# Kernel optimization log

Hardware: AMD Instinct MI355X
Metric: run time of the kernel (lower is better)

## Reference

```python
import jax, jax.numpy as jnp
import numpy as np

N = 50000
IN_DIM = 128
HEADS = 4
HEAD_DIM = IN_DIM // HEADS
TYPE_NUM = 3
E = 800000
NEG_SLOPE = 0.2


def setup_inputs() -> dict:
    key = jax.random.key(0)
    k1, k2, k3, k4, k5 = jax.random.split(key, 5)
    embedding = jax.random.normal(k1, (N, IN_DIM), dtype=jnp.float32)
    edges = jax.random.randint(k2, (TYPE_NUM, 2, E), 0, N, dtype=jnp.int32)
    W = jax.random.normal(k3, (TYPE_NUM, IN_DIM, HEADS, HEAD_DIM), dtype=jnp.float32) * 0.05
    a_src = jax.random.normal(k4, (TYPE_NUM, HEADS, HEAD_DIM), dtype=jnp.float32) * 0.05
    a_dst = jax.random.normal(k5, (TYPE_NUM, HEADS, HEAD_DIM), dtype=jnp.float32) * 0.05
    return {"embedding": embedding, "edges": edges, "W": W, "a_src": a_src, "a_dst": a_dst}


def _gat_layer(x, ei, W_t, asrc_t, adst_t):
    # x: [N, IN_DIM]; ei: [2, E]; W_t: [IN_DIM, H, D]
    h = jnp.einsum('nd,dhk->nhk', x, W_t)                  # [N, H, D]
    e_src = jnp.sum(h * asrc_t, axis=-1)                   # [N, H]
    e_dst = jnp.sum(h * adst_t, axis=-1)                   # [N, H]
    src, dst = ei[0], ei[1]
    e = jax.nn.leaky_relu(e_src[src] + e_dst[dst], NEG_SLOPE)  # [E, H]
    m = jax.ops.segment_max(e, dst, num_segments=N)        # [N, H]
    e = jnp.exp(e - m[dst])
    denom = jax.ops.segment_sum(e, dst, num_segments=N)    # [N, H]
    msg = h[src] * e[:, :, None]                           # [E, H, D]
    agg = jax.ops.segment_sum(msg, dst, num_segments=N)    # [N, H, D]
    out = agg / (denom[:, :, None] + 1e-9)
    return jax.nn.elu(out.reshape(N, HEADS * HEAD_DIM))


def reference(embedding, edges, W, a_src, a_dst):
    features_gat = [_gat_layer(embedding, edges[i], W[i], a_src[i], a_dst[i])
                    for i in range(TYPE_NUM)]
    # NOTE: the original module (faithfully) also uses the GAT layers for the
    # 'gcn' branch: features_gcn = [self.gat_layers[i](...) for ...]
    features_gcn = [_gat_layer(embedding, edges[i], W[i], a_src[i], a_dst[i])
                    for i in range(TYPE_NUM)]
    return (jnp.stack(features_gat), jnp.stack(features_gcn))
```

## Files before the change

kernel.cpp:

```cpp
#include <hip/hip_runtime.h>
#include <hip/hip_fp16.h>
#include <math.h>

#define NN 50000
#define IND 128
#define NH 4
#define NE 800000
#define NT 3
#define NSLOPE 0.2f

#define TILE 64
#define NBPT 782
#define NBTOT (NT * NBPT)
#define BCAP 1280

typedef _Float16 f16x8 __attribute__((ext_vector_type(8)));
typedef _Float16 f16x4 __attribute__((ext_vector_type(4)));
typedef float    f32x4 __attribute__((ext_vector_type(4)));

__global__ __launch_bounds__(256) void wt_prep_kernel(
    const float* __restrict__ W, __half* __restrict__ wt16g)
{
    int idx = blockIdx.x * 256 + threadIdx.x;
    if (idx >= NT * IND * IND) return;
    int t = idx / (IND * IND), r = idx - t * (IND * IND);
    int k = r >> 7, c = r & 127;
    wt16g[((size_t)t * IND + c) * IND + k] = (__half)W[idx];
}

__global__ __launch_bounds__(256) void gemm_mfma_kernel(
    const float* __restrict__ x, const __half* __restrict__ wt16g,
    const float* __restrict__ asrc, const float* __restrict__ adst,
    __half* __restrict__ h16, float* __restrict__ es, float* __restrict__ ed)
{
    __shared__ __align__(16) __half tile[4][16 * 136];
    const int t = blockIdx.y;
    const int tid = threadIdx.x;
    const int wid = tid >> 6, lane = tid & 63;
    const int l15 = lane & 15, l4 = lane >> 4;
    const int r0 = blockIdx.x * 64 + wid * 16;
    const bool active = (r0 < NN);

    const __half* wt = wt16g + (size_t)t * IND * IND;
    const float* xrow = x + (size_t)((active ? r0 : 0) + l15) * IND;

    f32x4 acc[8];
    #pragma unroll
    for (int i = 0; i < 8; i++) acc[i] = (f32x4){0.f, 0.f, 0.f, 0.f};

    #pragma unroll
    for (int ks = 0; ks < 4; ks++) {
        const int kb = ks * 32 + l4 * 8;
        float4 x0 = *reinterpret_cast<const float4*>(xrow + kb);
        float4 x1 = *reinterpret_cast<const float4*>(xrow + kb + 4);
        f16x8 af;
        af[0] = (_Float16)x0.x; af[1] = (_Float16)x0.y;
        af[2] = (_Float16)x0.z; af[3] = (_Float16)x0.w;
        af[4] = (_Float16)x1.x; af[5] = (_Float16)x1.y;
        af[6] = (_Float16)x1.z; af[7] = (_Float16)x1.w;
        #pragma unroll
        for (int ct = 0; ct < 8; ct++) {
            f16x8 bf = *reinterpret_cast<const f16x8*>(wt + (size_t)(ct * 16 + l15) * IND + kb);
            acc[ct] = __builtin_amdgcn_mfma_f32_16x16x32_f16(af, bf, acc[ct], 0, 0, 0);
        }
    }

    __half* tl = tile[wid];
    #pragma unroll
    for (int ct = 0; ct < 8; ct++)
        #pragma unroll
        for (int r = 0; r < 4; r++)
            tl[(l4 * 4 + r) * 136 + ct * 16 + l15] = (__half)acc[ct][r];
    __syncthreads();

    if (active) {
        #pragma unroll
        for (int i = 0; i < 4; i++) {
            int c = lane + 64 * i;
            int row = c >> 4, off = (c & 15) * 8;
            f16x8 v = *reinterpret_cast<const f16x8*>(tl + row * 136 + off);
            *reinterpret_cast<f16x8*>(h16 + ((size_t)t * NN + r0 + row) * IND + off) = v;
        }
        int row16 = lane >> 2, head = lane & 3;
        const __half* hr = tl + row16 * 136 + head * 32;
        const float* av = asrc + ((size_t)t * NH + head) * 32;
        const float* bv = adst + ((size_t)t * NH + head) * 32;
        float se = 0.f, de = 0.f;
        #pragma unroll
        for (int jj = 0; jj < 4; jj++) {
            f16x8 hv = *reinterpret_cast<const f16x8*>(hr + jj * 8);
            #pragma unroll
            for (int j = 0; j < 8; j++) {
                float hf = (float)hv[j];
                se = fmaf(hf, av[jj * 8 + j], se);
                de = fmaf(hf, bv[jj * 8 + j], de);
            }
        }
        int n = r0 + row16;
        es[((size_t)t * NN + n) * NH + head] = se;
        ed[((size_t)t * NN + n) * NH + head] = de;
    }
}

__global__ __launch_bounds__(256) void init_gcursor_kernel(int* __restrict__ gcursor)
{
    int i = blockIdx.x * 256 + threadIdx.x;
    if (i < NBTOT) gcursor[i] = i * BCAP;
}

__global__ __launch_bounds__(512) void bucket_scatter_kernel(
    const int* __restrict__ edges, int* __restrict__ gcursor, unsigned* __restrict__ bucketed)
{
    __shared__ int cnt[NBTOT];
    __shared__ int base[NBTOT];
    const int tid = threadIdx.x;
    for (int i = tid; i < NBTOT; i += 512) cnt[i] = 0;
    __syncthreads();
    const long long gtot = (long long)NT * NE;
    const long long g0 = (long long)blockIdx.x * 8192;
    long long g1 = g0 + 8192; if (g1 > gtot) g1 = gtot;
    for (long long g = g0 + tid; g < g1; g += 512) {
        int t = (g >= 2LL * NE) ? 2 : (g >= NE ? 1 : 0);
        int e = (int)(g - (long long)t * NE);
        int d = edges[(size_t)t * 2 * NE + NE + e];
        atomicAdd(&cnt[t * NBPT + (d >> 6)], 1);
    }
    __syncthreads();
    for (int i = tid; i < NBTOT; i += 512) {
        int c = cnt[i];
        base[i] = c ? atomicAdd(&gcursor[i], c) : 0;
        cnt[i] = 0;
    }
    __syncthreads();
    for (long long g = g0 + tid; g < g1; g += 512) {
        int t = (g >= 2LL * NE) ? 2 : (g >= NE ? 1 : 0);
        int e = (int)(g - (long long)t * NE);
        const int* eb = edges + (size_t)t * 2 * NE;
        int s = eb[e], d = eb[NE + e];
        int bg = t * NBPT + (d >> 6);
        int pos = base[bg] + atomicAdd(&cnt[bg], 1);
        bucketed[pos] = (unsigned)s | ((unsigned)(d & 63) << 16);
    }
}

__global__ __launch_bounds__(512) void bucket_sort_kernel(
    unsigned* __restrict__ bucketed, const int* __restrict__ gcursor,
    int* __restrict__ begA, int* __restrict__ endA)
{
    __shared__ unsigned pk[BCAP];
    __shared__ unsigned srt[BCAP];
    __shared__ int hist[TILE];
    __shared__ int scn[TILE];
    __shared__ int cur[TILE];
    const int bg = blockIdx.x;
    const int tid = threadIdx.x;
    const int base = bg * BCAP;
    const int cnt = gcursor[bg] - base;
    if (tid < TILE) { hist[tid] = 0; cur[tid] = 0; }
    __syncthreads();
    for (int i = tid; i < cnt; i += 512) {
        unsigned v = bucketed[base + i];
        pk[i] = v;
        atomicAdd(&hist[(v >> 16) & 63u], 1);
    }
    __syncthreads();
    if (tid < 64) {
        int v = hist[tid];
        int inc = v;
        #pragma unroll
        for (int off = 1; off < 64; off <<= 1) {
            int n = __shfl_up(inc, off, 64);
            if (tid >= off) inc += n;
        }
        scn[tid] = inc - v;
    }
    __syncthreads();
    for (int i = tid; i < cnt; i += 512) {
        unsigned v = pk[i];
        int dl = (int)((v >> 16) & 63u);
        int pos = scn[dl] + atomicAdd(&cur[dl], 1);
        srt[pos] = v & 0xFFFFu;
    }
    __syncthreads();
    for (int i = tid; i < cnt; i += 512) bucketed[base + i] = srt[i];
    if (tid < 64) {
        int t = bg / NBPT;
        int node = (bg - t * NBPT) * TILE + tid;
        if (node < NN) {
            int g = t * NN + node;
            begA[g] = base + scn[tid];
            endA[g] = base + scn[tid] + hist[tid];
        }
    }
}

__global__ __launch_bounds__(256) void gat_fused_kernel(
    const int* __restrict__ begA, const int* __restrict__ endA,
    const unsigned* __restrict__ ssrc,
    const float* __restrict__ es, const float* __restrict__ ed,
    const __half* __restrict__ h16,
    float* __restrict__ out)
{
    const int g = blockIdx.x * 4 + (threadIdx.x >> 6);
    if (g >= NT * NN) return;
    const int lane = threadIdx.x & 63;
    const int t = g / NN;
    const int dst = g - t * NN;
    const int beg = begA[g], end = endA[g];
    const int el = lane >> 5, dl = lane & 31;
    const int hsel = dl >> 3;
    const float* es_t = es + (size_t)t * NN * NH;
    const float edv = ed[(size_t)g * NH + (lane & 3)];
    const __half* h16_t = h16 + (size_t)t * NN * IND;

    float a0 = 0.f, a1 = 0.f, a2 = 0.f, a3 = 0.f, dsum = 0.f;

    for (int base = beg; base < end; base += 16) {
        int ne = end - base; if (ne > 16) ne = 16;
        const int ei = lane >> 2;
        float wv = 0.f; int sv = 0;
        if (ei < ne) {
            sv = (int)ssrc[base + ei];
            float s = es_t[(sv << 2) + (lane & 3)] + edv;
            s = s > 0.f ? s : NSLOPE * s;
            wv = __expf(s);
            dsum += wv;
        }
        int kk = 0;
        for (; kk + 2 <= ne; kk += 2) {
            int k2 = kk + el;
            int   sb = __shfl(sv, k2 << 2, 64);
            float wb = __shfl(wv, (k2 << 2) | hsel, 64);
            f16x4 hv = *reinterpret_cast<const f16x4*>(h16_t + ((size_t)sb << 7) + (dl << 2));
            a0 = fmaf(wb, (float)hv[0], a0);
            a1 = fmaf(wb, (float)hv[1], a1);
            a2 = fmaf(wb, (float)hv[2], a2);
            a3 = fmaf(wb, (float)hv[3], a3);
        }
        if (kk < ne) {
            int   sb = __shfl(sv, kk << 2, 64);
            float wb = __shfl(wv, (kk << 2) | hsel, 64);
            if (el == 0) {
                f16x4 hv = *reinterpret_cast<const f16x4*>(h16_t + ((size_t)sb << 7) + (dl << 2));
                a0 = fmaf(wb, (float)hv[0], a0);
                a1 = fmaf(wb, (float)hv[1], a1);
                a2 = fmaf(wb, (float)hv[2], a2);
                a3 = fmaf(wb, (float)hv[3], a3);
            }
        }
    }

    #pragma unroll
    for (int m = 4; m <= 32; m <<= 1) dsum += __shfl_xor(dsum, m, 64);
    a0 += __shfl_xor(a0, 32, 64);
    a1 += __shfl_xor(a1, 32, 64);
    a2 += __shfl_xor(a2, 32, 64);
    a3 += __shfl_xor(a3, 32, 64);
    float dn = __shfl(dsum, hsel, 64) + 1e-9f;

    if (el == 0) {
        float v0 = a0 / dn, v1 = a1 / dn, v2 = a2 / dn, v3 = a3 / dn;
        f32x4 o;
        o[0] = v0 > 0.f ? v0 : expm1f(v0);
        o[1] = v1 > 0.f ? v1 : expm1f(v1);
        o[2] = v2 > 0.f ? v2 : expm1f(v2);
        o[3] = v3 > 0.f ? v3 : expm1f(v3);
        float* obase = out + (size_t)t * NN * IND + ((size_t)dst << 7) + (dl << 2);
        __builtin_nontemporal_store(o, reinterpret_cast<f32x4*>(obase));
        __builtin_nontemporal_store(o, reinterpret_cast<f32x4*>(obase + (size_t)NT * NN * IND));
    }
}

extern "C" void kernel_launch(void* const* d_in, const int* in_sizes, int n_in,
                              void* d_out, int out_size, void* d_ws, size_t ws_size,
                              hipStream_t stream)
{
    const float* x     = (const float*)d_in[0];
    const int*   edges = (const int*)d_in[1];
    const float* W     = (const float*)d_in[2];
    const float* asrc  = (const float*)d_in[3];
    const float* adst  = (const float*)d_in[4];
    float* out = (float*)d_out;

    char* p = (char*)d_ws;
    __half*   h16      = (__half*)p;   p += (size_t)NT * NN * IND * 2;
    float*    es       = (float*)p;    p += (size_t)NT * NN * NH * 4;
    float*    ed       = (float*)p;    p += (size_t)NT * NN * NH * 4;
    int*      gcursor  = (int*)p;      p += (size_t)NBTOT * 4;
    int*      begA     = (int*)p;      p += (size_t)NT * NN * 4;
    int*      endA     = (int*)p;      p += (size_t)NT * NN * 4;
    __half*   wt16g    = (__half*)p;   p += (size_t)NT * IND * IND * 2;
    unsigned* bucketed = (unsigned*)p; p += ((size_t)NBTOT * BCAP + 1024) * 4;

    wt_prep_kernel<<<(NT * IND * IND + 255) / 256, 256, 0, stream>>>(W, wt16g);
    init_gcursor_kernel<<<(NBTOT + 255) / 256, 256, 0, stream>>>(gcursor);
    bucket_scatter_kernel<<<(NT * NE + 8191) / 8192, 512, 0, stream>>>(edges, gcursor, bucketed);
    bucket_sort_kernel<<<NBTOT, 512, 0, stream>>>(bucketed, gcursor, begA, endA);

    dim3 ggrid((NN + 63) / 64, NT);
    gemm_mfma_kernel<<<ggrid, 256, 0, stream>>>(x, wt16g, asrc, adst, h16, es, ed);

    gat_fused_kernel<<<(NT * NN + 3) / 4, 256, 0, stream>>>(
        begA, endA, bucketed, es, ed, h16, out);
}
```

Baseline: 247.5 us.

## Fuse kernels: merge prep, run scatter alongside GEMM, sort-and-aggregate per bucket

Cuts the launch count from six to three. Weight prep and cursor init now share one kernel. The edge bucket scatter and the MFMA GEMM run as disjoint block ranges of a single launch, so they can overlap. The bucket sort is fused with the GAT aggregation, so sorted source indices stay in LDS and no begin/end arrays are written or read back from global memory. The aggregation also uses inline v_fma_mix_f32 to fold the fp16-to-fp32 conversion into the FMA. In exchange, each 512-thread block now processes 64 destination nodes serially, eight per wave, which may reduce parallelism and hurt load balance on degree-skewed buckets.

```diff
diff --git a/kernel.cpp b/kernel.cpp
--- a/kernel.cpp
+++ b/kernel.cpp
@@ -14,31 +14,74 @@
 #define NBTOT (NT * NBPT)
 #define BCAP 1280
 
+#define SCB ((NT * NE + 8191) / 8192)
+#define GXB ((NN + 127) / 128)
+
 typedef _Float16 f16x8 __attribute__((ext_vector_type(8)));
-typedef _Float16 f16x4 __attribute__((ext_vector_type(4)));
 typedef float    f32x4 __attribute__((ext_vector_type(4)));
 
-__global__ __launch_bounds__(256) void wt_prep_kernel(
-    const float* __restrict__ W, __half* __restrict__ wt16g)
+__global__ __launch_bounds__(256) void prep_kernel(
+    const float* __restrict__ W, __half* __restrict__ wt16g, int* __restrict__ gcursor)
 {
     int idx = blockIdx.x * 256 + threadIdx.x;
-    if (idx >= NT * IND * IND) return;
-    int t = idx / (IND * IND), r = idx - t * (IND * IND);
-    int k = r >> 7, c = r & 127;
-    wt16g[((size_t)t * IND + c) * IND + k] = (__half)W[idx];
-}
-
-__global__ __launch_bounds__(256) void gemm_mfma_kernel(
+    if (idx < NT * IND * IND) {
+        int t = idx / (IND * IND), r = idx - t * (IND * IND);
+        int k = r >> 7, c = r & 127;
+        wt16g[((size_t)t * IND + c) * IND + k] = (__half)W[idx];
+    }
+    if (idx < NBTOT) gcursor[idx] = idx * BCAP;
+}
+
+__global__ __launch_bounds__(512) void scatter_gemm_kernel(
+    const int* __restrict__ edges, int* __restrict__ gcursor, unsigned* __restrict__ bucketed,
     const float* __restrict__ x, const __half* __restrict__ wt16g,
     const float* __restrict__ asrc, const float* __restrict__ adst,
     __half* __restrict__ h16, float* __restrict__ es, float* __restrict__ ed)
 {
-    __shared__ __align__(16) __half tile[4][16 * 136];
-    const int t = blockIdx.y;
+    __shared__ __align__(16) char ldsbuf[34816];
     const int tid = threadIdx.x;
+
+    if (blockIdx.x < SCB) {
+        int* cnt = (int*)ldsbuf;
+        int* bas = cnt + NBTOT;
+        for (int i = tid; i < NBTOT; i += 512) cnt[i] = 0;
+        __syncthreads();
+        const long long gtot = (long long)NT * NE;
+        const long long g0 = (long long)blockIdx.x * 8192;
+        long long g1 = g0 + 8192; if (g1 > gtot) g1 = gtot;
+        for (long long g = g0 + tid; g < g1; g += 512) {
+            int t = (g >= 2LL * NE) ? 2 : (g >= NE ? 1 : 0);
+            int e = (int)(g - (long long)t * NE);
+            int d = edges[(size_t)t * 2 * NE + NE + e];
+            atomicAdd(&cnt[t * NBPT + (d >> 6)], 1);
+        }
+        __syncthreads();
+        for (int i = tid; i < NBTOT; i += 512) {
+            int c = cnt[i];
+            bas[i] = c ? atomicAdd(&gcursor[i], c) : 0;
+            cnt[i] = 0;
+        }
+        __syncthreads();
+        for (long long g = g0 + tid; g < g1; g += 512) {
+            int t = (g >= 2LL * NE) ? 2 : (g >= NE ? 1 : 0);
+            int e = (int)(g - (long long)t * NE);
+            const int* eb = edges + (size_t)t * 2 * NE;
+            int s = eb[e], d = eb[NE + e];
+            int bg = t * NBPT + (d >> 6);
+            int pos = bas[bg] + atomicAdd(&cnt[bg], 1);
+            bucketed[pos] = (unsigned)s | ((unsigned)(d & 63) << 16);
+        }
+        return;
+    }
+
+    const int bx = blockIdx.x - SCB;
+    const int t  = bx / GXB;
+    const int gx = bx - t * GXB;
+    __half* tile = (__half*)ldsbuf;
     const int wid = tid >> 6, lane = tid & 63;
+    __half* tl = tile + wid * (16 * 136);
     const int l15 = lane & 15, l4 = lane >> 4;
-    const int r0 = blockIdx.x * 64 + wid * 16;
+    const int r0 = gx * 128 + wid * 16;
     const bool active = (r0 < NN);
 
     const __half* wt = wt16g + (size_t)t * IND * IND;
@@ -65,7 +108,6 @@
         }
     }
 
-    __half* tl = tile[wid];
     #pragma unroll
     for (int ct = 0; ct < 8; ct++)
         #pragma unroll
@@ -102,60 +144,21 @@
     }
 }
 
-__global__ __launch_bounds__(256) void init_gcursor_kernel(int* __restrict__ gcursor)
-{
-    int i = blockIdx.x * 256 + threadIdx.x;
-    if (i < NBTOT) gcursor[i] = i * BCAP;
-}
-
-__global__ __launch_bounds__(512) void bucket_scatter_kernel(
-    const int* __restrict__ edges, int* __restrict__ gcursor, unsigned* __restrict__ bucketed)
-{
-    __shared__ int cnt[NBTOT];
-    __shared__ int base[NBTOT];
-    const int tid = threadIdx.x;
-    for (int i = tid; i < NBTOT; i += 512) cnt[i] = 0;
-    __syncthreads();
-    const long long gtot = (long long)NT * NE;
-    const long long g0 = (long long)blockIdx.x * 8192;
-    long long g1 = g0 + 8192; if (g1 > gtot) g1 = gtot;
-    for (long long g = g0 + tid; g < g1; g += 512) {
-        int t = (g >= 2LL * NE) ? 2 : (g >= NE ? 1 : 0);
-        int e = (int)(g - (long long)t * NE);
-        int d = edges[(size_t)t * 2 * NE + NE + e];
-        atomicAdd(&cnt[t * NBPT + (d >> 6)], 1);
-    }
-    __syncthreads();
-    for (int i = tid; i < NBTOT; i += 512) {
-        int c = cnt[i];
-        base[i] = c ? atomicAdd(&gcursor[i], c) : 0;
-        cnt[i] = 0;
-    }
-    __syncthreads();
-    for (long long g = g0 + tid; g < g1; g += 512) {
-        int t = (g >= 2LL * NE) ? 2 : (g >= NE ? 1 : 0);
-        int e = (int)(g - (long long)t * NE);
-        const int* eb = edges + (size_t)t * 2 * NE;
-        int s = eb[e], d = eb[NE + e];
-        int bg = t * NBPT + (d >> 6);
-        int pos = base[bg] + atomicAdd(&cnt[bg], 1);
-        bucketed[pos] = (unsigned)s | ((unsigned)(d & 63) << 16);
-    }
-}
-
-__global__ __launch_bounds__(512) void bucket_sort_kernel(
-    unsigned* __restrict__ bucketed, const int* __restrict__ gcursor,
-    int* __restrict__ begA, int* __restrict__ endA)
+__global__ __launch_bounds__(512) void gat_bucket_kernel(
+    const unsigned* __restrict__ bucketed, const int* __restrict__ gcursor,
+    const float* __restrict__ es, const float* __restrict__ ed,
+    const __half* __restrict__ h16, float* __restrict__ out)
 {
     __shared__ unsigned pk[BCAP];
     __shared__ unsigned srt[BCAP];
-    __shared__ int hist[TILE];
-    __shared__ int scn[TILE];
-    __shared__ int cur[TILE];
+    __shared__ int hist[TILE], scn[TILE], cur[TILE];
     const int bg = blockIdx.x;
+    const int t = bg / NBPT;
+    const int node0 = (bg - t * NBPT) * TILE;
     const int tid = threadIdx.x;
     const int base = bg * BCAP;
     const int cnt = gcursor[bg] - base;
+
     if (tid < TILE) { hist[tid] = 0; cur[tid] = 0; }
     __syncthreads();
     for (int i = tid; i < cnt; i += 512) {
@@ -182,92 +185,76 @@
         srt[pos] = v & 0xFFFFu;
     }
     __syncthreads();
-    for (int i = tid; i < cnt; i += 512) bucketed[base + i] = srt[i];
-    if (tid < 64) {
-        int t = bg / NBPT;
-        int node = (bg - t * NBPT) * TILE + tid;
-        if (node < NN) {
-            int g = t * NN + node;
-            begA[g] = base + scn[tid];
-            endA[g] = base + scn[tid] + hist[tid];
-        }
-    }
-}
-
-__global__ __launch_bounds__(256) void gat_fused_kernel(
-    const int* __restrict__ begA, const int* __restrict__ endA,
-    const unsigned* __restrict__ ssrc,
-    const float* __restrict__ es, const float* __restrict__ ed,
-    const __half* __restrict__ h16,
-    float* __restrict__ out)
-{
-    const int g = blockIdx.x * 4 + (threadIdx.x >> 6);
-    if (g >= NT * NN) return;
-    const int lane = threadIdx.x & 63;
-    const int t = g / NN;
-    const int dst = g - t * NN;
-    const int beg = begA[g], end = endA[g];
-    const int el = lane >> 5, dl = lane & 31;
-    const int hsel = dl >> 3;
+
+    const int wid = tid >> 6, lane = tid & 63;
+    const int el = lane >> 5, dl2 = lane & 31;
+    const int hsel = dl2 >> 3;
     const float* es_t = es + (size_t)t * NN * NH;
-    const float edv = ed[(size_t)g * NH + (lane & 3)];
     const __half* h16_t = h16 + (size_t)t * NN * IND;
 
-    float a0 = 0.f, a1 = 0.f, a2 = 0.f, a3 = 0.f, dsum = 0.f;
-
-    for (int base = beg; base < end; base += 16) {
-        int ne = end - base; if (ne > 16) ne = 16;
-        const int ei = lane >> 2;
-        float wv = 0.f; int sv = 0;
-        if (ei < ne) {
-            sv = (int)ssrc[base + ei];
-            float s = es_t[(sv << 2) + (lane & 3)] + edv;
-            s = s > 0.f ? s : NSLOPE * s;
-            wv = __expf(s);
-            dsum += wv;
-        }
-        int kk = 0;
-        for (; kk + 2 <= ne; kk += 2) {
-            int k2 = kk + el;
-            int   sb = __shfl(sv, k2 << 2, 64);
-            float wb = __shfl(wv, (k2 << 2) | hsel, 64);
-            f16x4 hv = *reinterpret_cast<const f16x4*>(h16_t + ((size_t)sb << 7) + (dl << 2));
-            a0 = fmaf(wb, (float)hv[0], a0);
-            a1 = fmaf(wb, (float)hv[1], a1);
-            a2 = fmaf(wb, (float)hv[2], a2);
-            a3 = fmaf(wb, (float)hv[3], a3);
-        }
-        if (kk < ne) {
-            int   sb = __shfl(sv, kk << 2, 64);
-            float wb = __shfl(wv, (kk << 2) | hsel, 64);
-            if (el == 0) {
-                f16x4 hv = *reinterpret_cast<const f16x4*>(h16_t + ((size_t)sb << 7) + (dl << 2));
-                a0 = fmaf(wb, (float)hv[0], a0);
-                a1 = fmaf(wb, (float)hv[1], a1);
-                a2 = fmaf(wb, (float)hv[2], a2);
-                a3 = fmaf(wb, (float)hv[3], a3);
-            }
-        }
-    }
-
-    #pragma unroll
-    for (int m = 4; m <= 32; m <<= 1) dsum += __shfl_xor(dsum, m, 64);
-    a0 += __shfl_xor(a0, 32, 64);
-    a1 += __shfl_xor(a1, 32, 64);
-    a2 += __shfl_xor(a2, 32, 64);
-    a3 += __shfl_xor(a3, 32, 64);
-    float dn = __shfl(dsum, hsel, 64) + 1e-9f;
-
-    if (el == 0) {
-        float v0 = a0 / dn, v1 = a1 / dn, v2 = a2 / dn, v3 = a3 / dn;
-        f32x4 o;
-        o[0] = v0 > 0.f ? v0 : expm1f(v0);
-        o[1] = v1 > 0.f ? v1 : expm1f(v1);
-        o[2] = v2 > 0.f ? v2 : expm1f(v2);
-        o[3] = v3 > 0.f ? v3 : expm1f(v3);
-        float* obase = out + (size_t)t * NN * IND + ((size_t)dst << 7) + (dl << 2);
-        __builtin_nontemporal_store(o, reinterpret_cast<f32x4*>(obase));
-        __builtin_nontemporal_store(o, reinterpret_cast<f32x4*>(obase + (size_t)NT * NN * IND));
+    for (int j = 0; j < 8; j++) {
+        const int dloc = wid * 8 + j;
+        const int node = node0 + dloc;
+        if (node >= NN) break;
+        const int beg = scn[dloc], nE = hist[dloc];
+        const float edv = ed[((size_t)t * NN + node) * NH + (lane & 3)];
+
+        float a0 = 0.f, a1 = 0.f, a2 = 0.f, a3 = 0.f, dsum = 0.f;
+
+        for (int b2 = 0; b2 < nE; b2 += 16) {
+            int ne = nE - b2; if (ne > 16) ne = 16;
+            const int ei = lane >> 2;
+            float wv = 0.f; int sv = 0;
+            if (ei < ne) {
+                sv = (int)srt[beg + b2 + ei];
+                float s = es_t[(sv << 2) + (lane & 3)] + edv;
+                s = s > 0.f ? s : NSLOPE * s;
+                wv = __expf(s);
+                dsum += wv;
+            }
+            int kk = 0;
+            for (; kk + 2 <= ne; kk += 2) {
+                int k2 = kk + el;
+                int   sb = __shfl(sv, k2 << 2, 64);
+                float wb = __shfl(wv, (k2 << 2) | hsel, 64);
+                uint2 hv = *reinterpret_cast<const uint2*>(h16_t + ((size_t)sb << 7) + (dl2 << 2));
+                asm("v_fma_mix_f32 %0, %1, %2, %0 op_sel:[0,0,0] op_sel_hi:[1,0,0]" : "+v"(a0) : "v"(hv.x), "v"(wb));
+                asm("v_fma_mix_f32 %0, %1, %2, %0 op_sel:[1,0,0] op_sel_hi:[1,0,0]" : "+v"(a1) : "v"(hv.x), "v"(wb));
+                asm("v_fma_mix_f32 %0, %1, %2, %0 op_sel:[0,0,0] op_sel_hi:[1,0,0]" : "+v"(a2) : "v"(hv.y), "v"(wb));
+                asm("v_fma_mix_f32 %0, %1, %2, %0 op_sel:[1,0,0] op_sel_hi:[1,0,0]" : "+v"(a3) : "v"(hv.y), "v"(wb));
+            }
+            if (kk < ne) {
+                int   sb = __shfl(sv, kk << 2, 64);
+                float wb = __shfl(wv, (kk << 2) | hsel, 64);
+                if (el == 0) {
+                    uint2 hv = *reinterpret_cast<const uint2*>(h16_t + ((size_t)sb << 7) + (dl2 << 2));
+                    asm("v_fma_mix_f32 %0, %1, %2, %0 op_sel:[0,0,0] op_sel_hi:[1,0,0]" : "+v"(a0) : "v"(hv.x), "v"(wb));
+                    asm("v_fma_mix_f32 %0, %1, %2, %0 op_sel:[1,0,0] op_sel_hi:[1,0,0]" : "+v"(a1) : "v"(hv.x), "v"(wb));
+                    asm("v_fma_mix_f32 %0, %1, %2, %0 op_sel:[0,0,0] op_sel_hi:[1,0,0]" : "+v"(a2) : "v"(hv.y), "v"(wb));
+                    asm("v_fma_mix_f32 %0, %1, %2, %0 op_sel:[1,0,0] op_sel_hi:[1,0,0]" : "+v"(a3) : "v"(hv.y), "v"(wb));
+                }
+            }
+        }
+
+        #pragma unroll
+        for (int m = 4; m <= 32; m <<= 1) dsum += __shfl_xor(dsum, m, 64);
+        a0 += __shfl_xor(a0, 32, 64);
+        a1 += __shfl_xor(a1, 32, 64);
+        a2 += __shfl_xor(a2, 32, 64);
+        a3 += __shfl_xor(a3, 32, 64);
+        float dn = __shfl(dsum, hsel, 64) + 1e-9f;
+
+        if (el == 0) {
+            float v0 = a0 / dn, v1 = a1 / dn, v2 = a2 / dn, v3 = a3 / dn;
+            f32x4 o;
+            o[0] = v0 > 0.f ? v0 : expm1f(v0);
+            o[1] = v1 > 0.f ? v1 : expm1f(v1);
+            o[2] = v2 > 0.f ? v2 : expm1f(v2);
+            o[3] = v3 > 0.f ? v3 : expm1f(v3);
+            float* obase = out + (size_t)t * NN * IND + ((size_t)node << 7) + (dl2 << 2);
+            __builtin_nontemporal_store(o, reinterpret_cast<f32x4*>(obase));
+            __builtin_nontemporal_store(o, reinterpret_cast<f32x4*>(obase + (size_t)NT * NN * IND));
+        }
     }
 }
 
@@ -287,19 +274,11 @@
     float*    es       = (float*)p;    p += (size_t)NT * NN * NH * 4;
     float*    ed       = (float*)p;    p += (size_t)NT * NN * NH * 4;
     int*      gcursor  = (int*)p;      p += (size_t)NBTOT * 4;
-    int*      begA     = (int*)p;      p += (size_t)NT * NN * 4;
-    int*      endA     = (int*)p;      p += (size_t)NT * NN * 4;
     __half*   wt16g    = (__half*)p;   p += (size_t)NT * IND * IND * 2;
     unsigned* bucketed = (unsigned*)p; p += ((size_t)NBTOT * BCAP + 1024) * 4;
 
-    wt_prep_kernel<<<(NT * IND * IND + 255) / 256, 256, 0, stream>>>(W, wt16g);
-    init_gcursor_kernel<<<(NBTOT + 255) / 256, 256, 0, stream>>>(gcursor);
-    bucket_scatter_kernel<<<(NT * NE + 8191) / 8192, 512, 0, stream>>>(edges, gcursor, bucketed);
-    bucket_sort_kernel<<<NBTOT, 512, 0, stream>>>(bucketed, gcursor, begA, endA);
-
-    dim3 ggrid((NN + 63) / 64, NT);
-    gemm_mfma_kernel<<<ggrid, 256, 0, stream>>>(x, wt16g, asrc, adst, h16, es, ed);
-
-    gat_fused_kernel<<<(NT * NN + 3) / 4, 256, 0, stream>>>(
-        begA, endA, bucketed, es, ed, h16, out);
-}
+    prep_kernel<<<(NT * IND * IND + 255) / 256, 256, 0, stream>>>(W, wt16g, gcursor);
+    scatter_gemm_kernel<<<SCB + NT * GXB, 512, 0, stream>>>(
+        edges, gcursor, bucketed, x, wt16g, asrc, adst, h16, es, ed);
+    gat_bucket_kernel<<<NBTOT, 512, 0, stream>>>(bucketed, gcursor, es, ed, h16, out);
+}
```

Result: faster. 226.5 us (-8.5%).
